# Optimization experiments

Measured on AMD Instinct MI355X. Metric: run time of the kernel, lower is better.

The kernel has to match this reference:

```python
import jax, jax.numpy as jnp
import numpy as np
import math

N, IN_DIM, Z, H, OUT, K = 16384, 64, 128, 1, 3, 16


def setup_inputs() -> dict:
    key = jax.random.key(0)
    ks = jax.random.split(key, 16)

    def lin(k, din, dout):
        kw, kb = jax.random.split(k)
        W = jax.random.normal(kw, (din, dout), jnp.float32) / math.sqrt(din)
        b = jax.random.normal(kb, (dout,), jnp.float32) * 0.01
        return W, b

    x = jax.random.normal(ks[0], (N, IN_DIM), jnp.float32)
    t = jnp.zeros((1,), jnp.float32)
    # layer dims: (in, heads*out) per TransformerConv
    dims = [(IN_DIM, Z * H), (Z * H, (Z // H) * H), (Z * H, (OUT // H) * H)]
    params = {}
    i = 1
    for li, (din, dout) in enumerate(dims, 1):
        for nm in ("q", "k", "v", "s"):
            W, b = lin(ks[i], din, dout)
            i += 1
            params[f"W{nm}{li}"] = W
            params[f"b{nm}{li}"] = b
    return {"t": t, "x": x, **params}


def knn_edge_index(coo, k):
    # kNN graph on 3-D coords (loop=False): edges neighbor(src) -> center(dst)
    n = coo.shape[0]
    sq = jnp.sum(coo * coo, axis=-1)
    d = sq[:, None] + sq[None, :] - 2.0 * (coo @ coo.T)  # [N, N] sq. distances
    d = d.at[jnp.arange(n), jnp.arange(n)].set(jnp.inf)  # exclude self-loops
    _, idx = jax.lax.top_k(-d, k)  # [N, K] nearest neighbor indices
    src = idx.reshape(-1)
    dst = jnp.repeat(jnp.arange(n), k)
    return src, dst


def tconv(x, src, dst, Wq, bq, Wk, bk, Wv, bv, Ws, bs, heads):
    # PyG TransformerConv (concat=True, root_weight=True, no edge_attr)
    n = x.shape[0]
    dout = Wq.shape[1]
    c = dout // heads
    q = (x @ Wq + bq).reshape(n, heads, c)
    kk = (x @ Wk + bk).reshape(n, heads, c)
    v = (x @ Wv + bv).reshape(n, heads, c)
    alpha = jnp.sum(q[dst] * kk[src], axis=-1) / math.sqrt(c)  # [E, H]
    amax = jax.ops.segment_max(alpha, dst, num_segments=n)
    ex = jnp.exp(alpha - amax[dst])
    denom = jax.ops.segment_sum(ex, dst, num_segments=n)
    w = ex / denom[dst]  # softmax over incoming edges per node
    msg = w[:, :, None] * v[src]  # [E, H, C]
    out = jax.ops.segment_sum(msg, dst, num_segments=n).reshape(n, dout)
    return out + x @ Ws + bs  # root/skip connection


def reference(t, x,
              Wq1, bq1, Wk1, bk1, Wv1, bv1, Ws1, bs1,
              Wq2, bq2, Wk2, bk2, Wv2, bv2, Ws2, bs2,
              Wq3, bq3, Wk3, bk3, Wv3, bv3, Ws3, bs3):
    src, dst = knn_edge_index(x[:, :3], K)  # built under no_grad in original
    h = jnp.tanh(tconv(x, src, dst, Wq1, bq1, Wk1, bk1, Wv1, bv1, Ws1, bs1, H))
    h = jnp.tanh(tconv(h, src, dst, Wq2, bq2, Wk2, bk2, Wv2, bv2, Ws2, bs2, H) + h)
    drift_coo = tconv(h, src, dst, Wq3, bq3, Wk3, bk3, Wv3, bv3, Ws3, bs3, H)
    return drift_coo
```

## Files before the change

kernel.cpp:

```cpp
#include <hip/hip_runtime.h>
#include <math.h>

#define NN 16384
#define QPW 2
#define CAP 128
#define WM 64
#define KTOP 17

typedef unsigned long long u64;

__global__ __launch_bounds__(256) void pack_coords(const float* __restrict__ x,
                                                   float4* __restrict__ coo) {
  int i = blockIdx.x * 256 + threadIdx.x;
  float a = x[i * 64 + 0];
  float b = x[i * 64 + 1];
  float c = x[i * 64 + 2];
  coo[i] = make_float4(a, b, c, a * a + b * b + c * c);
}

__device__ __forceinline__ int mbcnt64(u64 mask) {
  return __builtin_amdgcn_mbcnt_hi(
      (unsigned)(mask >> 32),
      __builtin_amdgcn_mbcnt_lo((unsigned)mask, 0));
}

__device__ __forceinline__ unsigned fmap(float d) {
  unsigned ub = __float_as_uint(d);
  return ub ^ ((unsigned)((int)ub >> 31) | 0x80000000u);
}

__device__ __forceinline__ float unfmap(unsigned ub) {
  unsigned fb = (ub & 0x80000000u) ? (ub ^ 0x80000000u) : ~ub;
  return __uint_as_float(fb);
}

__device__ __forceinline__ u64 u64min(u64 a, u64 b) { return a < b ? a : b; }
__device__ __forceinline__ u64 u64max(u64 a, u64 b) { return a > b ? a : b; }

__device__ __forceinline__ void sort128(u64& r0, u64& r1, int lane) {
#pragma unroll
  for (int k = 2; k <= 128; k <<= 1) {
    if (k == 128) {
      u64 lo = u64min(r0, r1);
      r1 = u64max(r0, r1);
      r0 = lo;
    }
#pragma unroll
    for (int jj = (k == 128 ? 32 : (k >> 1)); jj >= 1; jj >>= 1) {
      const bool up = (lane & jj) == 0;
      const bool asc0 = (lane & k) == 0;
      const bool asc1 = ((lane | 64) & k) == 0;
      u64 o0 = __shfl_xor(r0, jj);
      u64 o1 = __shfl_xor(r1, jj);
      r0 = (up == asc0) ? u64min(r0, o0) : u64max(r0, o0);
      r1 = (up == asc1) ? u64min(r1, o1) : u64max(r1, o1);
    }
  }
}

__device__ __forceinline__ void radix_shrink(u64* buf, int& cnt, float& th,
                                             int lane) {
  const u64 k0 = (lane < cnt) ? buf[lane] : ~0ull;
  const u64 k1 = (lane + 64 < cnt) ? buf[lane + 64] : ~0ull;
  const unsigned d0 = (unsigned)(k0 >> 32);
  const unsigned d1 = (unsigned)(k1 >> 32);
  unsigned p = 0u;
#pragma unroll
  for (int b = 31; b >= 0; --b) {
    const unsigned c = p | (1u << b);
    const u64 b0 = __ballot(d0 < c);
    const u64 b1 = __ballot(d1 < c);
    const int n = __popcll(b0) + __popcll(b1);
    if (n < KTOP) p = c;
  }
  const bool v0 = d0 <= p;
  const bool v1 = d1 <= p;
  const u64 m0 = __ballot(v0);
  const u64 m1 = __ballot(v1);
  const int base = __popcll(m0);
  if (v0) buf[mbcnt64(m0)] = k0;
  if (v1) buf[base + mbcnt64(m1)] = k1;
  cnt = base + __popcll(m1);
  th = unfmap(p);
}

__global__ __launch_bounds__(256) void knn_kernel(const float4* __restrict__ coo,
                                                  int* __restrict__ src) {
  __shared__ u64 bufs[4][QPW][CAP];
  const int lane = threadIdx.x & 63;
  const int wid = threadIdx.x >> 6;
  const int node0 = blockIdx.x * (4 * QPW) + wid * QPW;

  float nx[QPW], ny[QPW], nz[QPW], sq[QPW], th[QPW];
  int cnt[QPW];
#pragma unroll
  for (int q = 0; q < QPW; ++q) {
    const float4 me = coo[node0 + q];
    nx[q] = -2.0f * me.x;
    ny[q] = -2.0f * me.y;
    nz[q] = -2.0f * me.z;
    sq[q] = me.w;
    cnt[q] = 0;
  }

  {
    const float4 pa = coo[lane];
    const float4 pb = coo[64 + lane];
#pragma unroll
    for (int q = 0; q < QPW; ++q) {
      const float d0 = sq[q] + fmaf(nx[q], pa.x,
                           fmaf(ny[q], pa.y, fmaf(nz[q], pa.z, pa.w)));
      const float d1 = sq[q] + fmaf(nx[q], pb.x,
                           fmaf(ny[q], pb.y, fmaf(nz[q], pb.z, pb.w)));
      bufs[wid][q][lane] = ((u64)fmap(d0) << 32) | (unsigned)lane;
      bufs[wid][q][64 + lane] = ((u64)fmap(d1) << 32) | (unsigned)(64 + lane);
      cnt[q] = 128;
      radix_shrink(bufs[wid][q], cnt[q], th[q], lane);
    }
  }

  float4 s0 = coo[2 * 64 + lane];
  float4 s1 = coo[3 * 64 + lane];
  float4 s2 = coo[4 * 64 + lane];
  float4 s3 = coo[5 * 64 + lane];

  auto body = [&](const float4 cur, const int step) {
    const int j = step * 64 + lane;
    float dd[QPW];
#pragma unroll
    for (int q = 0; q < QPW; ++q)
      dd[q] = sq[q] + fmaf(nx[q], cur.x,
                           fmaf(ny[q], cur.y, fmaf(nz[q], cur.z, cur.w)));
    u64 mk[QPW];
#pragma unroll
    for (int q = 0; q < QPW; ++q) mk[q] = __ballot(dd[q] <= th[q]);
    if (mk[0] | mk[1]) {
#pragma unroll
      for (int q = 0; q < QPW; ++q) {
        if (mk[q]) {
          if (dd[q] <= th[q])
            bufs[wid][q][cnt[q] + mbcnt64(mk[q])] =
                ((u64)fmap(dd[q]) << 32) | (unsigned)j;
          cnt[q] += __popcll(mk[q]);
          if (cnt[q] >= WM) radix_shrink(bufs[wid][q], cnt[q], th[q], lane);
        }
      }
    }
  };

#pragma unroll 1
  for (int g = 0; g < 63; ++g) {
    const int base = 2 + g * 4;
    body(s0, base + 0);
    s0 = coo[(base + 4) * 64 + lane];
    body(s1, base + 1);
    s1 = coo[(base + 5) * 64 + lane];
    body(s2, base + 2);
    s2 = coo[(base + 6) * 64 + lane];
    body(s3, base + 3);
    s3 = coo[(base + 7) * 64 + lane];
  }
  body(s0, 254);
  body(s1, 255);

#pragma unroll 1
  for (int q = 0; q < QPW; ++q) {
    u64 r0 = (lane < cnt[q]) ? bufs[wid][q][lane] : ~0ull;
    u64 r1 = (lane + 64 < cnt[q]) ? bufs[wid][q][lane + 64] : ~0ull;
    sort128(r0, r1, lane);
    const int idx = (int)(r0 & 0xFFFFFFFFull);
    const u64 selfm = __ballot((lane < KTOP) && (idx == node0 + q));
    const int s = selfm ? (__ffsll((long long)selfm) - 1) : 99;
    const int outrank = lane - (lane > s ? 1 : 0);
    if (lane < KTOP && lane != s && outrank < 16)
      src[(node0 + q) * 16 + outrank] = idx;
  }
}

template <int KD>
__global__ __launch_bounds__(256) void gemm_qkvs(
    const float* __restrict__ X, const float* __restrict__ W0,
    const float* __restrict__ W1, const float* __restrict__ W2,
    const float* __restrict__ W3, const float* __restrict__ B0,
    const float* __restrict__ B1, const float* __restrict__ B2,
    const float* __restrict__ B3, float* __restrict__ out) {
  __shared__ float As[64][68];
  __shared__ float Bs[64][64];
  const int brow = blockIdx.x * 64;
  const int by = blockIdx.y;
  const int wi = by >> 1;
  const float* W = wi == 0 ? W0 : wi == 1 ? W1 : wi == 2 ? W2 : W3;
  const float* bias = wi == 0 ? B0 : wi == 1 ? B1 : wi == 2 ? B2 : B3;
  const int cbase = (by & 1) * 64;
  const int tx = threadIdx.x & 15;
  const int ty = threadIdx.x >> 4;

  float acc[4][4] = {};
  for (int k0 = 0; k0 < KD; k0 += 64) {
    __syncthreads();
#pragma unroll
    for (int i = 0; i < 4; ++i) {
      const int flat = threadIdx.x * 4 + i * 1024;
      const int r = flat >> 6, kk = flat & 63;
      const float4 v = *(const float4*)&X[(brow + r) * KD + k0 + kk];
      As[kk + 0][r] = v.x;
      As[kk + 1][r] = v.y;
      As[kk + 2][r] = v.z;
      As[kk + 3][r] = v.w;
    }
#pragma unroll
    for (int i = 0; i < 4; ++i) {
      const int flat = threadIdx.x * 4 + i * 1024;
      const int kk = flat >> 6, c = flat & 63;
      *(float4*)&Bs[kk][c] = *(const float4*)&W[(k0 + kk) * 128 + cbase + c];
    }
    __syncthreads();
#pragma unroll 8
    for (int k = 0; k < 64; ++k) {
      const float4 a = *(const float4*)&As[k][ty * 4];
      const float4 b = *(const float4*)&Bs[k][tx * 4];
      const float av[4] = {a.x, a.y, a.z, a.w};
      const float bv[4] = {b.x, b.y, b.z, b.w};
#pragma unroll
      for (int i = 0; i < 4; ++i)
#pragma unroll
        for (int jj = 0; jj < 4; ++jj)
          acc[i][jj] = fmaf(av[i], bv[jj], acc[i][jj]);
    }
  }
  const float4 bi = *(const float4*)&bias[cbase + tx * 4];
#pragma unroll
  for (int i = 0; i < 4; ++i) {
    const int row = brow + ty * 4 + i;
    float4 o;
    o.x = acc[i][0] + bi.x;
    o.y = acc[i][1] + bi.y;
    o.z = acc[i][2] + bi.z;
    o.w = acc[i][3] + bi.w;
    *(float4*)&out[row * 512 + wi * 128 + cbase + tx * 4] = o;
  }
}

__global__ __launch_bounds__(256) void attn_c128(
    const float* __restrict__ qkvs, const int* __restrict__ src,
    const float* __restrict__ res, float* __restrict__ hout, int do_res) {
  const int g = threadIdx.x >> 5;
  const int node = blockIdx.x * 8 + g;
  const int c = threadIdx.x & 31;
  const float4 q4 = ((const float4*)(qkvs + node * 512))[c];

  int nb[16];
#pragma unroll
  for (int r = 0; r < 16; ++r) nb[r] = src[node * 16 + r];

  float p[16];
#pragma unroll
  for (int r = 0; r < 16; ++r) {
    const float4 k4 = ((const float4*)(qkvs + nb[r] * 512 + 128))[c];
    p[r] = q4.x * k4.x + q4.y * k4.y + q4.z * k4.z + q4.w * k4.w;
  }
#pragma unroll
  for (int o = 16; o; o >>= 1) {
#pragma unroll
    for (int r = 0; r < 16; ++r) p[r] += __shfl_xor(p[r], o);
  }

  float m = p[0];
#pragma unroll
  for (int r = 1; r < 16; ++r) m = fmaxf(m, p[r]);
  float w[16];
  float den = 0.0f;
#pragma unroll
  for (int r = 0; r < 16; ++r) {
    w[r] = __expf((p[r] - m) * 0.088388347648318447f);
    den += w[r];
  }
  const float inv = 1.0f / den;
  float o0 = 0.0f, o1 = 0.0f, o2 = 0.0f, o3 = 0.0f;
#pragma unroll
  for (int r = 0; r < 16; ++r) {
    const float4 v4 = ((const float4*)(qkvs + nb[r] * 512 + 256))[c];
    const float ww = w[r] * inv;
    o0 = fmaf(ww, v4.x, o0);
    o1 = fmaf(ww, v4.y, o1);
    o2 = fmaf(ww, v4.z, o2);
    o3 = fmaf(ww, v4.w, o3);
  }
  const float4 s4 = ((const float4*)(qkvs + node * 512 + 384))[c];
  float r0 = o0 + s4.x, r1 = o1 + s4.y, r2 = o2 + s4.z, r3 = o3 + s4.w;
  if (do_res) {
    const float4 h4 = ((const float4*)(res + node * 128))[c];
    r0 += h4.x;
    r1 += h4.y;
    r2 += h4.z;
    r3 += h4.w;
  }
  ((float4*)(hout + node * 128))[c] =
      make_float4(tanhf(r0), tanhf(r1), tanhf(r2), tanhf(r3));
}

__global__ __launch_bounds__(256) void gemm_qkvs3(
    const float* __restrict__ H, const float* __restrict__ W0,
    const float* __restrict__ W1, const float* __restrict__ W2,
    const float* __restrict__ W3, const float* __restrict__ B0,
    const float* __restrict__ B1, const float* __restrict__ B2,
    const float* __restrict__ B3, float* __restrict__ out) {
  __shared__ float hs[64][132];
  __shared__ float wsh[128 * 12];
  __shared__ float bsh[12];
  const int brow = blockIdx.x * 64;
  if (threadIdx.x < 12) {
    const int mi = threadIdx.x / 3, c = threadIdx.x % 3;
    const float* Bsel = mi == 0 ? B0 : mi == 1 ? B1 : mi == 2 ? B2 : B3;
    bsh[threadIdx.x] = Bsel[c];
  }
  for (int t = threadIdx.x; t < 1536; t += 256) {
    const int k = t / 12, cc = t % 12;
    const int mi = cc / 3, c = cc % 3;
    const float* Wsel = mi == 0 ? W0 : mi == 1 ? W1 : mi == 2 ? W2 : W3;
    wsh[t] = Wsel[k * 3 + c];
  }
#pragma unroll
  for (int i = 0; i < 8; ++i) {
    const int flat = threadIdx.x * 4 + i * 1024;
    const int r = flat >> 7, kk = flat & 127;
    *(float4*)&hs[r][kk] = *(const float4*)&H[(brow + r) * 128 + kk];
  }
  __syncthreads();
  const int r = threadIdx.x >> 2;
  const int part = threadIdx.x & 3;
  float a0 = 0.0f, a1 = 0.0f, a2 = 0.0f;
#pragma unroll 4
  for (int k = 0; k < 128; ++k) {
    const float h = hs[r][k];
    a0 = fmaf(h, wsh[k * 12 + part * 3 + 0], a0);
    a1 = fmaf(h, wsh[k * 12 + part * 3 + 1], a1);
    a2 = fmaf(h, wsh[k * 12 + part * 3 + 2], a2);
  }
  const int row = brow + r;
  out[row * 12 + part * 3 + 0] = a0 + bsh[part * 3 + 0];
  out[row * 12 + part * 3 + 1] = a1 + bsh[part * 3 + 1];
  out[row * 12 + part * 3 + 2] = a2 + bsh[part * 3 + 2];
}

__global__ __launch_bounds__(256) void attn_c3(const float* __restrict__ q3,
                                               const int* __restrict__ src,
                                               float* __restrict__ out) {
  const int gid = blockIdx.x * 256 + threadIdx.x;
  const int node = gid >> 4, r = gid & 15;
  const int j = src[node * 16 + r];
  const float* qn = q3 + node * 12;
  const float* kj = q3 + j * 12 + 3;
  float alpha = (qn[0] * kj[0] + qn[1] * kj[1] + qn[2] * kj[2]) *
                0.57735026918962576f;
  float m = alpha;
#pragma unroll
  for (int o = 8; o; o >>= 1) m = fmaxf(m, __shfl_xor(m, o, 16));
  const float e = __expf(alpha - m);
  float den = e;
#pragma unroll
  for (int o = 8; o; o >>= 1) den += __shfl_xor(den, o, 16);
  const float wgt = e / den;
  const float* vj = q3 + j * 12 + 6;
  float o0 = wgt * vj[0], o1 = wgt * vj[1], o2 = wgt * vj[2];
#pragma unroll
  for (int o = 8; o; o >>= 1) {
    o0 += __shfl_xor(o0, o, 16);
    o1 += __shfl_xor(o1, o, 16);
    o2 += __shfl_xor(o2, o, 16);
  }
  if (r == 0) {
    const float* sn = q3 + node * 12 + 9;
    out[node * 3 + 0] = o0 + sn[0];
    out[node * 3 + 1] = o1 + sn[1];
    out[node * 3 + 2] = o2 + sn[2];
  }
}

extern "C" void kernel_launch(void* const* d_in, const int* in_sizes, int n_in,
                              void* d_out, int out_size, void* d_ws,
                              size_t ws_size, hipStream_t stream) {
  const float* x = (const float*)d_in[1];
  const float* Wq1 = (const float*)d_in[2];
  const float* bq1 = (const float*)d_in[3];
  const float* Wk1 = (const float*)d_in[4];
  const float* bk1 = (const float*)d_in[5];
  const float* Wv1 = (const float*)d_in[6];
  const float* bv1 = (const float*)d_in[7];
  const float* Ws1 = (const float*)d_in[8];
  const float* bs1 = (const float*)d_in[9];
  const float* Wq2 = (const float*)d_in[10];
  const float* bq2 = (const float*)d_in[11];
  const float* Wk2 = (const float*)d_in[12];
  const float* bk2 = (const float*)d_in[13];
  const float* Wv2 = (const float*)d_in[14];
  const float* bv2 = (const float*)d_in[15];
  const float* Ws2 = (const float*)d_in[16];
  const float* bs2 = (const float*)d_in[17];
  const float* Wq3 = (const float*)d_in[18];
  const float* bq3 = (const float*)d_in[19];
  const float* Wk3 = (const float*)d_in[20];
  const float* bk3 = (const float*)d_in[21];
  const float* Wv3 = (const float*)d_in[22];
  const float* bv3 = (const float*)d_in[23];
  const float* Ws3 = (const float*)d_in[24];
  const float* bs3 = (const float*)d_in[25];

  char* ws = (char*)d_ws;
  float* qkvs = (float*)(ws);
  float* h1 = (float*)(ws + (size_t)32 * 1024 * 1024);
  float* h2 = (float*)(ws + (size_t)40 * 1024 * 1024);
  int* src = (int*)(ws + (size_t)48 * 1024 * 1024);
  float4* coo = (float4*)(ws + (size_t)49 * 1024 * 1024);
  float* q3 = (float*)(ws + (size_t)49 * 1024 * 1024 + 512 * 1024);
  float* out = (float*)d_out;

  pack_coords<<<NN / 256, 256, 0, stream>>>(x, coo);
  knn_kernel<<<NN / (4 * QPW), 256, 0, stream>>>(coo, src);
  gemm_qkvs<64><<<dim3(NN / 64, 8), 256, 0, stream>>>(
      x, Wq1, Wk1, Wv1, Ws1, bq1, bk1, bv1, bs1, qkvs);
  attn_c128<<<NN / 8, 256, 0, stream>>>(qkvs, src, nullptr, h1, 0);
  gemm_qkvs<128><<<dim3(NN / 64, 8), 256, 0, stream>>>(
      h1, Wq2, Wk2, Wv2, Ws2, bq2, bk2, bv2, bs2, qkvs);
  attn_c128<<<NN / 8, 256, 0, stream>>>(qkvs, src, h1, h2, 1);
  gemm_qkvs3<<<NN / 64, 256, 0, stream>>>(h2, Wq3, Wk3, Wv3, Ws3, bq3, bk3,
                                          bv3, bs3, q3);
  attn_c3<<<NN * 16 / 256, 256, 0, stream>>>(q3, src, out);
}
```

Measured before the change: 336.8 us.

## Split kNN scan into two halves with merge, store K/V in bf16

The kNN kernel now splits each node's candidate scan into two halves run by separate blocks. Each half writes its 17 best keys to a partial buffer, and a new merge kernel sorts the 34 candidates and drops the self index. This doubles the number of blocks, giving more parallelism and shorter per-wave serial loops. Separately, the layer-1/2 GEMMs store K and V as bf16, which halves the gather traffic in the attention kernels at the cost of reduced precision in attention scores and messages.

```diff
diff --git a/kernel.cpp b/kernel.cpp
--- a/kernel.cpp
+++ b/kernel.cpp
@@ -32,6 +32,14 @@
 __device__ __forceinline__ float unfmap(unsigned ub) {
   unsigned fb = (ub & 0x80000000u) ? (ub ^ 0x80000000u) : ~ub;
   return __uint_as_float(fb);
+}
+
+__device__ __forceinline__ unsigned short f2bf(float f) {
+  unsigned u = __float_as_uint(f);
+  return (unsigned short)((u + 0x7FFFu + ((u >> 16) & 1u)) >> 16);
+}
+__device__ __forceinline__ float bf2f(unsigned short h) {
+  return __uint_as_float(((unsigned)h) << 16);
 }
 
 __device__ __forceinline__ u64 u64min(u64 a, u64 b) { return a < b ? a : b; }
@@ -84,12 +92,14 @@
   th = unfmap(p);
 }
 
-__global__ __launch_bounds__(256) void knn_kernel(const float4* __restrict__ coo,
-                                                  int* __restrict__ src) {
+__global__ __launch_bounds__(256) void knn_part(const float4* __restrict__ coo,
+                                                u64* __restrict__ part) {
   __shared__ u64 bufs[4][QPW][CAP];
   const int lane = threadIdx.x & 63;
   const int wid = threadIdx.x >> 6;
-  const int node0 = blockIdx.x * (4 * QPW) + wid * QPW;
+  const int half = blockIdx.x & 1;
+  const int node0 = (blockIdx.x >> 1) * (4 * QPW) + wid * QPW;
+  const int cb = half * 128;
 
   float nx[QPW], ny[QPW], nz[QPW], sq[QPW], th[QPW];
   int cnt[QPW];
@@ -104,28 +114,29 @@
   }
 
   {
-    const float4 pa = coo[lane];
-    const float4 pb = coo[64 + lane];
+    const float4 pa = coo[cb * 64 + lane];
+    const float4 pb = coo[cb * 64 + 64 + lane];
 #pragma unroll
     for (int q = 0; q < QPW; ++q) {
       const float d0 = sq[q] + fmaf(nx[q], pa.x,
                            fmaf(ny[q], pa.y, fmaf(nz[q], pa.z, pa.w)));
       const float d1 = sq[q] + fmaf(nx[q], pb.x,
                            fmaf(ny[q], pb.y, fmaf(nz[q], pb.z, pb.w)));
-      bufs[wid][q][lane] = ((u64)fmap(d0) << 32) | (unsigned)lane;
-      bufs[wid][q][64 + lane] = ((u64)fmap(d1) << 32) | (unsigned)(64 + lane);
+      bufs[wid][q][lane] = ((u64)fmap(d0) << 32) | (unsigned)(cb * 64 + lane);
+      bufs[wid][q][64 + lane] =
+          ((u64)fmap(d1) << 32) | (unsigned)(cb * 64 + 64 + lane);
       cnt[q] = 128;
       radix_shrink(bufs[wid][q], cnt[q], th[q], lane);
     }
   }
 
-  float4 s0 = coo[2 * 64 + lane];
-  float4 s1 = coo[3 * 64 + lane];
-  float4 s2 = coo[4 * 64 + lane];
-  float4 s3 = coo[5 * 64 + lane];
-
-  auto body = [&](const float4 cur, const int step) {
-    const int j = step * 64 + lane;
+  float4 s0 = coo[(cb + 2) * 64 + lane];
+  float4 s1 = coo[(cb + 3) * 64 + lane];
+  float4 s2 = coo[(cb + 4) * 64 + lane];
+  float4 s3 = coo[(cb + 5) * 64 + lane];
+
+  auto body = [&](const float4 cur, const int rel) {
+    const int j = (cb + rel) * 64 + lane;
     float dd[QPW];
 #pragma unroll
     for (int q = 0; q < QPW; ++q)
@@ -149,32 +160,42 @@
   };
 
 #pragma unroll 1
-  for (int g = 0; g < 63; ++g) {
+  for (int g = 0; g < 31; ++g) {
     const int base = 2 + g * 4;
     body(s0, base + 0);
-    s0 = coo[(base + 4) * 64 + lane];
+    s0 = coo[(cb + base + 4) * 64 + lane];
     body(s1, base + 1);
-    s1 = coo[(base + 5) * 64 + lane];
+    s1 = coo[(cb + base + 5) * 64 + lane];
     body(s2, base + 2);
-    s2 = coo[(base + 6) * 64 + lane];
+    s2 = coo[(cb + base + 6) * 64 + lane];
     body(s3, base + 3);
-    s3 = coo[(base + 7) * 64 + lane];
-  }
-  body(s0, 254);
-  body(s1, 255);
+    s3 = coo[(cb + base + 7) * 64 + lane];
+  }
+  body(s0, 126);
+  body(s1, 127);
 
 #pragma unroll 1
   for (int q = 0; q < QPW; ++q) {
     u64 r0 = (lane < cnt[q]) ? bufs[wid][q][lane] : ~0ull;
     u64 r1 = (lane + 64 < cnt[q]) ? bufs[wid][q][lane + 64] : ~0ull;
     sort128(r0, r1, lane);
-    const int idx = (int)(r0 & 0xFFFFFFFFull);
-    const u64 selfm = __ballot((lane < KTOP) && (idx == node0 + q));
-    const int s = selfm ? (__ffsll((long long)selfm) - 1) : 99;
-    const int outrank = lane - (lane > s ? 1 : 0);
-    if (lane < KTOP && lane != s && outrank < 16)
-      src[(node0 + q) * 16 + outrank] = idx;
-  }
+    if (lane < KTOP) part[(node0 + q) * 34 + half * 17 + lane] = r0;
+  }
+}
+
+__global__ __launch_bounds__(256) void knn_merge(const u64* __restrict__ part,
+                                                 int* __restrict__ src) {
+  const int lane = threadIdx.x & 63;
+  const int wid = threadIdx.x >> 6;
+  const int node = blockIdx.x * 4 + wid;
+  u64 r0 = (lane < 34) ? part[node * 34 + lane] : ~0ull;
+  u64 r1 = ~0ull;
+  sort128(r0, r1, lane);
+  const int idx = (int)(r0 & 0xFFFFFFFFull);
+  const u64 selfm = __ballot((lane < KTOP) && (idx == node));
+  const int s = selfm ? (__ffsll((long long)selfm) - 1) : 99;
+  const int outrank = lane - (lane > s ? 1 : 0);
+  if (lane < KTOP && lane != s && outrank < 16) src[node * 16 + outrank] = idx;
 }
 
 template <int KD>
@@ -183,7 +204,8 @@
     const float* __restrict__ W1, const float* __restrict__ W2,
     const float* __restrict__ W3, const float* __restrict__ B0,
     const float* __restrict__ B1, const float* __restrict__ B2,
-    const float* __restrict__ B3, float* __restrict__ out) {
+    const float* __restrict__ B3, float* __restrict__ qs,
+    unsigned short* __restrict__ kvh) {
   __shared__ float As[64][68];
   __shared__ float Bs[64][64];
   const int brow = blockIdx.x * 64;
@@ -229,6 +251,7 @@
     }
   }
   const float4 bi = *(const float4*)&bias[cbase + tx * 4];
+  const int col = cbase + tx * 4;
 #pragma unroll
   for (int i = 0; i < 4; ++i) {
     const int row = brow + ty * 4 + i;
@@ -237,17 +260,29 @@
     o.y = acc[i][1] + bi.y;
     o.z = acc[i][2] + bi.z;
     o.w = acc[i][3] + bi.w;
-    *(float4*)&out[row * 512 + wi * 128 + cbase + tx * 4] = o;
+    if (wi == 0) {
+      *(float4*)&qs[row * 256 + col] = o;
+    } else if (wi == 3) {
+      *(float4*)&qs[row * 256 + 128 + col] = o;
+    } else {
+      ushort4 h;
+      h.x = f2bf(o.x);
+      h.y = f2bf(o.y);
+      h.z = f2bf(o.z);
+      h.w = f2bf(o.w);
+      *(ushort4*)&kvh[row * 256 + (wi == 1 ? col : 128 + col)] = h;
+    }
   }
 }
 
 __global__ __launch_bounds__(256) void attn_c128(
-    const float* __restrict__ qkvs, const int* __restrict__ src,
-    const float* __restrict__ res, float* __restrict__ hout, int do_res) {
+    const float* __restrict__ qs, const unsigned short* __restrict__ kvh,
+    const int* __restrict__ src, const float* __restrict__ res,
+    float* __restrict__ hout, int do_res) {
   const int g = threadIdx.x >> 5;
   const int node = blockIdx.x * 8 + g;
   const int c = threadIdx.x & 31;
-  const float4 q4 = ((const float4*)(qkvs + node * 512))[c];
+  const float4 q4 = ((const float4*)(qs + node * 256))[c];
 
   int nb[16];
 #pragma unroll
@@ -256,8 +291,9 @@
   float p[16];
 #pragma unroll
   for (int r = 0; r < 16; ++r) {
-    const float4 k4 = ((const float4*)(qkvs + nb[r] * 512 + 128))[c];
-    p[r] = q4.x * k4.x + q4.y * k4.y + q4.z * k4.z + q4.w * k4.w;
+    const ushort4 k4 = ((const ushort4*)(kvh + nb[r] * 256))[c];
+    p[r] = q4.x * bf2f(k4.x) + q4.y * bf2f(k4.y) + q4.z * bf2f(k4.z) +
+           q4.w * bf2f(k4.w);
   }
 #pragma unroll
   for (int o = 16; o; o >>= 1) {
@@ -279,14 +315,14 @@
   float o0 = 0.0f, o1 = 0.0f, o2 = 0.0f, o3 = 0.0f;
 #pragma unroll
   for (int r = 0; r < 16; ++r) {
-    const float4 v4 = ((const float4*)(qkvs + nb[r] * 512 + 256))[c];
+    const ushort4 v4 = ((const ushort4*)(kvh + nb[r] * 256 + 128))[c];
     const float ww = w[r] * inv;
-    o0 = fmaf(ww, v4.x, o0);
-    o1 = fmaf(ww, v4.y, o1);
-    o2 = fmaf(ww, v4.z, o2);
-    o3 = fmaf(ww, v4.w, o3);
-  }
-  const float4 s4 = ((const float4*)(qkvs + node * 512 + 384))[c];
+    o0 = fmaf(ww, bf2f(v4.x), o0);
+    o1 = fmaf(ww, bf2f(v4.y), o1);
+    o2 = fmaf(ww, bf2f(v4.z), o2);
+    o3 = fmaf(ww, bf2f(v4.w), o3);
+  }
+  const float4 s4 = ((const float4*)(qs + node * 256 + 128))[c];
   float r0 = o0 + s4.x, r1 = o1 + s4.y, r2 = o2 + s4.z, r3 = o3 + s4.w;
   if (do_res) {
     const float4 h4 = ((const float4*)(res + node * 128))[c];
@@ -406,23 +442,27 @@
   const float* Ws3 = (const float*)d_in[24];
   const float* bs3 = (const float*)d_in[25];
 
+  const size_t MB = 1024 * 1024;
   char* ws = (char*)d_ws;
-  float* qkvs = (float*)(ws);
-  float* h1 = (float*)(ws + (size_t)32 * 1024 * 1024);
-  float* h2 = (float*)(ws + (size_t)40 * 1024 * 1024);
-  int* src = (int*)(ws + (size_t)48 * 1024 * 1024);
-  float4* coo = (float4*)(ws + (size_t)49 * 1024 * 1024);
-  float* q3 = (float*)(ws + (size_t)49 * 1024 * 1024 + 512 * 1024);
+  float* qs = (float*)(ws);
+  u64* part = (u64*)(ws);
+  unsigned short* kvh = (unsigned short*)(ws + 16 * MB);
+  float* h1 = (float*)(ws + 24 * MB);
+  float* h2 = (float*)(ws + 32 * MB);
+  int* src = (int*)(ws + 40 * MB);
+  float4* coo = (float4*)(ws + 41 * MB);
+  float* q3 = (float*)(ws + 42 * MB);
   float* out = (float*)d_out;
 
   pack_coords<<<NN / 256, 256, 0, stream>>>(x, coo);
-  knn_kernel<<<NN / (4 * QPW), 256, 0, stream>>>(coo, src);
+  knn_part<<<NN / (4 * QPW) * 2, 256, 0, stream>>>(coo, part);
+  knn_merge<<<NN / 4, 256, 0, stream>>>(part, src);
   gemm_qkvs<64><<<dim3(NN / 64, 8), 256, 0, stream>>>(
-      x, Wq1, Wk1, Wv1, Ws1, bq1, bk1, bv1, bs1, qkvs);
-  attn_c128<<<NN / 8, 256, 0, stream>>>(qkvs, src, nullptr, h1, 0);
+      x, Wq1, Wk1, Wv1, Ws1, bq1, bk1, bv1, bs1, qs, kvh);
+  attn_c128<<<NN / 8, 256, 0, stream>>>(qs, kvh, src, nullptr, h1, 0);
   gemm_qkvs<128><<<dim3(NN / 64, 8), 256, 0, stream>>>(
-      h1, Wq2, Wk2, Wv2, Ws2, bq2, bk2, bv2, bs2, qkvs);
-  attn_c128<<<NN / 8, 256, 0, stream>>>(qkvs, src, h1, h2, 1);
+      h1, Wq2, Wk2, Wv2, Ws2, bq2, bk2, bv2, bs2, qs, kvh);
+  attn_c128<<<NN / 8, 256, 0, stream>>>(qs, kvh, src, h1, h2, 1);
   gemm_qkvs3<<<NN / 64, 256, 0, stream>>>(h2, Wq3, Wk3, Wv3, Ws3, bq3, bk3,
                                           bv3, bs3, q3);
   attn_c3<<<NN * 16 / 256, 256, 0, stream>>>(q3, src, out);
```

New measurement: 385.7 us. 14.5% more time.
